# Kernel tuning notes

Hardware: AMD Instinct MI355X
Metric: run time of the kernel (lower is better)

## Reference

```python
import jax, jax.numpy as jnp
import numpy as np

N = 50000      # nodes
E = 250000     # edges
NG = 2500      # graphs
H = 32         # atom_dim
ND = 32        # node feature dim
ED = 16        # edge feature dim
CONV_N = 3     # message passing steps
EMB_STEPS = 3  # Set2Set processing steps


def setup_inputs() -> dict:
    key = jax.random.key(0)
    ks = jax.random.split(key, 16)
    w = lambda k, shape, s=0.05: jax.random.normal(k, shape, jnp.float32) * s
    return {
        "x": jax.random.normal(ks[0], (N, ND), jnp.float32),
        "edge_index": jax.random.randint(ks[1], (2, E), 0, N),
        "edge_attr": jax.random.normal(ks[2], (E, ED), jnp.float32),
        "batch": jnp.sort(jax.random.randint(ks[3], (N,), 0, NG)),
        "lin_w": w(ks[4], (ND, H)), "lin_b": jnp.zeros((H,), jnp.float32),
        "e_w1": w(ks[5], (ED, 2 * H)), "e_b1": jnp.zeros((2 * H,), jnp.float32),
        "e_w2": w(ks[6], (2 * H, H * H)), "e_b2": jnp.zeros((H * H,), jnp.float32),
        "gru_w_ih": w(ks[7], (3 * H, H)), "gru_w_hh": w(ks[8], (3 * H, H)),
        "gru_b_ih": jnp.zeros((3 * H,), jnp.float32), "gru_b_hh": jnp.zeros((3 * H,), jnp.float32),
        "lstm_w_ih": w(ks[9], (4 * H, 2 * H)), "lstm_w_hh": w(ks[10], (4 * H, H)),
        "lstm_b_ih": jnp.zeros((4 * H,), jnp.float32), "lstm_b_hh": jnp.zeros((4 * H,), jnp.float32),
        "pred_w": w(ks[11], (2 * H, 1)), "pred_b": jnp.zeros((1,), jnp.float32),
    }


def _mpnn_forward(x, edge_attr, lin_w, lin_b, e_w1, e_b1, e_w2, e_b2,
                  gru_w_ih, gru_w_hh, gru_b_ih, gru_b_hh,
                  lstm_w_ih, lstm_w_hh, lstm_b_ih, lstm_b_hh,
                  pred_w, pred_b, edge_index, batch):
    src, dst = edge_index[0], edge_index[1]
    # initial node embedding: relu(Linear(node_dim -> atom_dim))
    out = jax.nn.relu(x @ lin_w + lin_b)            # [N, H]
    h = out                                         # GRU hidden state [N, H]

    # edge-conditioned weights (edge MLP output is constant across conv steps)
    e_h = jax.nn.relu(edge_attr @ e_w1 + e_b1)      # [E, 2H]
    W_e = (e_h @ e_w2 + e_b2).reshape(E, H, H)      # [E, H, H]

    # mean-aggregation denominator per target node
    deg = jax.ops.segment_sum(jnp.ones((E,), out.dtype), dst, num_segments=N)
    denom = jnp.maximum(deg, 1.0)[:, None]          # [N, 1]

    for _ in range(CONV_N):
        # NNConv message: m_e = x_src @ W_e, mean-scattered to dst
        msg = jnp.einsum('eh,eho->eo', out[src], W_e)                   # [E, H]
        agg = jax.ops.segment_sum(msg, dst, num_segments=N) / denom     # [N, H]
        m = jax.nn.relu(agg)
        # single GRU cell step (seq_len=1)
        gi = m @ gru_w_ih.T + gru_b_ih              # [N, 3H]
        gh = h @ gru_w_hh.T + gru_b_hh              # [N, 3H]
        i_r, i_z, i_n = jnp.split(gi, 3, axis=-1)
        h_r, h_z, h_n = jnp.split(gh, 3, axis=-1)
        r = jax.nn.sigmoid(i_r + h_r)
        z = jax.nn.sigmoid(i_z + h_z)
        n = jnp.tanh(i_n + r * h_n)
        h = (1.0 - z) * n + z * h
        out = h

    # Set2Set pooling over graphs (only last embedding used, residual='last')
    q_star = jnp.zeros((NG, 2 * H), out.dtype)
    hl = jnp.zeros((NG, H), out.dtype)
    cl = jnp.zeros((NG, H), out.dtype)
    for _ in range(EMB_STEPS):
        g = q_star @ lstm_w_ih.T + lstm_b_ih + hl @ lstm_w_hh.T + lstm_b_hh  # [NG, 4H]
        gi_, gf_, gg_, go_ = jnp.split(g, 4, axis=-1)
        i_g = jax.nn.sigmoid(gi_)
        f_g = jax.nn.sigmoid(gf_)
        g_g = jnp.tanh(gg_)
        o_g = jax.nn.sigmoid(go_)
        cl = f_g * cl + i_g * g_g
        hl = o_g * jnp.tanh(cl)
        q = hl                                       # [NG, H]
        e = jnp.sum(out * q[batch], axis=-1)         # [N]
        e_max = jax.ops.segment_max(e, batch, num_segments=NG)
        e_exp = jnp.exp(e - e_max[batch])
        e_den = jax.ops.segment_sum(e_exp, batch, num_segments=NG)
        a = e_exp / e_den[batch]                     # softmax within each graph
        r_pool = jax.ops.segment_sum(a[:, None] * out, batch, num_segments=NG)  # [NG, H]
        q_star = jnp.concatenate([q, r_pool], axis=-1)

    pred = q_star @ pred_w + pred_b                  # [NG, 1]
    return pred.reshape(-1)


def reference(x, edge_index, edge_attr, batch, lin_w, lin_b, e_w1, e_b1, e_w2, e_b2,
              gru_w_ih, gru_w_hh, gru_b_ih, gru_b_hh,
              lstm_w_ih, lstm_w_hh, lstm_b_ih, lstm_b_hh, pred_w, pred_b):
    return _mpnn_forward(x, edge_attr, lin_w, lin_b, e_w1, e_b1, e_w2, e_b2,
                         gru_w_ih, gru_w_hh, gru_b_ih, gru_b_hh,
                         lstm_w_ih, lstm_w_hh, lstm_b_ih, lstm_b_hh,
                         pred_w, pred_b, edge_index, batch)
```

## Files before the change

### kernel.cpp

```cpp
#include <hip/hip_runtime.h>
#include <hip/hip_bf16.h>

namespace {
constexpr int kN = 50000;
constexpr int kE = 250000;
constexpr int kG = 2500;
constexpr int NB = 8;
constexpr int NBLK = (kN + 255) / 256;

__device__ __forceinline__ float sigmoidf_(float x) { return 1.0f / (1.0f + expf(-x)); }

__global__ void k_starts(const int* __restrict__ batch, int* __restrict__ starts) {
  int g = blockIdx.x * blockDim.x + threadIdx.x;
  if (g > kG) return;
  int lo = 0, hi = kN;
  while (lo < hi) {
    int mid = (lo + hi) >> 1;
    if (batch[mid] < g) lo = mid + 1; else hi = mid;
  }
  starts[g] = lo;
}

__global__ __launch_bounds__(256) void k_node_init(const float* __restrict__ x,
                                                   const float* __restrict__ lin_w,
                                                   const float* __restrict__ lin_b,
                                                   float* __restrict__ h) {
  __shared__ float ws[32 * 32];
  __shared__ float bs[32];
  for (int i = threadIdx.x; i < 1024; i += 256) ws[i] = lin_w[i];
  if (threadIdx.x < 32) bs[threadIdx.x] = lin_b[threadIdx.x];
  __syncthreads();
  int n = blockIdx.x * 256 + threadIdx.x;
  if (n >= kN) return;
  float xv[32];
  const float4* xp = (const float4*)(x + (size_t)n * 32);
#pragma unroll
  for (int i = 0; i < 8; ++i) {
    float4 v = xp[i];
    xv[4 * i + 0] = v.x; xv[4 * i + 1] = v.y; xv[4 * i + 2] = v.z; xv[4 * i + 3] = v.w;
  }
  float acc[32];
#pragma unroll
  for (int o = 0; o < 32; ++o) acc[o] = bs[o];
  for (int i = 0; i < 32; ++i) {
    float a = xv[i];
    const float4* wr = (const float4*)&ws[i * 32];
#pragma unroll
    for (int o4 = 0; o4 < 8; ++o4) {
      float4 w = wr[o4];
      acc[4 * o4 + 0] = fmaf(a, w.x, acc[4 * o4 + 0]);
      acc[4 * o4 + 1] = fmaf(a, w.y, acc[4 * o4 + 1]);
      acc[4 * o4 + 2] = fmaf(a, w.z, acc[4 * o4 + 2]);
      acc[4 * o4 + 3] = fmaf(a, w.w, acc[4 * o4 + 3]);
    }
  }
  float4* hp = (float4*)(h + (size_t)n * 32);
#pragma unroll
  for (int i = 0; i < 8; ++i) {
    float4 v;
    v.x = fmaxf(acc[4 * i + 0], 0.f);
    v.y = fmaxf(acc[4 * i + 1], 0.f);
    v.z = fmaxf(acc[4 * i + 2], 0.f);
    v.w = fmaxf(acc[4 * i + 3], 0.f);
    hp[i] = v;
  }
}

__global__ __launch_bounds__(256) void k_edge_h(const float* __restrict__ ea,
                                                const float* __restrict__ w1,
                                                const float* __restrict__ b1,
                                                const int* __restrict__ es_e,
                                                float* __restrict__ ehs) {
  __shared__ float ws[16 * 64];
  __shared__ float bs[64];
  for (int i = threadIdx.x; i < 1024; i += 256) ws[i] = w1[i];
  if (threadIdx.x < 64) bs[threadIdx.x] = b1[threadIdx.x];
  __syncthreads();
  int pos = blockIdx.x * 256 + threadIdx.x;
  if (pos >= kE) return;
  int e = es_e[pos];
  float av[16];
  const float4* ap = (const float4*)(ea + (size_t)e * 16);
#pragma unroll
  for (int i = 0; i < 4; ++i) {
    float4 v = ap[i];
    av[4 * i + 0] = v.x; av[4 * i + 1] = v.y; av[4 * i + 2] = v.z; av[4 * i + 3] = v.w;
  }
  float acc[64];
#pragma unroll
  for (int o = 0; o < 64; ++o) acc[o] = bs[o];
  for (int i = 0; i < 16; ++i) {
    float a = av[i];
    const float4* wr = (const float4*)&ws[i * 64];
#pragma unroll
    for (int o4 = 0; o4 < 16; ++o4) {
      float4 w = wr[o4];
      acc[4 * o4 + 0] = fmaf(a, w.x, acc[4 * o4 + 0]);
      acc[4 * o4 + 1] = fmaf(a, w.y, acc[4 * o4 + 1]);
      acc[4 * o4 + 2] = fmaf(a, w.z, acc[4 * o4 + 2]);
      acc[4 * o4 + 3] = fmaf(a, w.w, acc[4 * o4 + 3]);
    }
  }
  float4* op = (float4*)(ehs + (size_t)pos * 64);
#pragma unroll
  for (int i = 0; i < 16; ++i) {
    float4 v;
    v.x = fmaxf(acc[4 * i + 0], 0.f);
    v.y = fmaxf(acc[4 * i + 1], 0.f);
    v.z = fmaxf(acc[4 * i + 2], 0.f);
    v.w = fmaxf(acc[4 * i + 3], 0.f);
    op[i] = v;
  }
}

__global__ void k_hist2(const int* __restrict__ src, const int* __restrict__ dst,
                        int* __restrict__ cnt_s, int* __restrict__ cnt_d) {
  int e = blockIdx.x * blockDim.x + threadIdx.x;
  if (e < kE) {
    atomicAdd(&cnt_s[src[e]], 1);
    atomicAdd(&cnt_d[dst[e]], 1);
  }
}

__global__ __launch_bounds__(256) void k_scan_blk(const int* __restrict__ cnt_s, int* __restrict__ offs_s,
                                                  const int* __restrict__ cnt_d, int* __restrict__ offs_d,
                                                  int* __restrict__ part) {
  const int arr = blockIdx.y;
  const int* cnt = arr ? cnt_d : cnt_s;
  int* offs = arr ? offs_d : offs_s;
  __shared__ int wsum[4];
  const int i = blockIdx.x * 256 + threadIdx.x;
  const int lane = threadIdx.x & 63, wv = threadIdx.x >> 6;
  int v = (i < kN) ? cnt[i] : 0;
  int x = v;
#pragma unroll
  for (int d = 1; d < 64; d <<= 1) {
    int t = __shfl_up(x, d, 64);
    if (lane >= d) x += t;
  }
  if (lane == 63) wsum[wv] = x;
  __syncthreads();
  int pre = 0;
#pragma unroll
  for (int w = 0; w < 3; ++w) pre += (w < wv) ? wsum[w] : 0;
  if (i < kN) offs[i] = pre + x - v;
  if (threadIdx.x == 255) part[arr * 256 + blockIdx.x] = pre + x;
}

__global__ __launch_bounds__(256) void k_scan_part(int* __restrict__ part,
                                                   int* __restrict__ offs_s,
                                                   int* __restrict__ offs_d) {
  const int arr = blockIdx.x;
  int* p = part + arr * 256;
  __shared__ int wsum[4];
  const int i = threadIdx.x;
  const int lane = i & 63, wv = i >> 6;
  int v = (i < NBLK) ? p[i] : 0;
  int x = v;
#pragma unroll
  for (int d = 1; d < 64; d <<= 1) {
    int t = __shfl_up(x, d, 64);
    if (lane >= d) x += t;
  }
  if (lane == 63) wsum[wv] = x;
  __syncthreads();
  int pre = 0;
#pragma unroll
  for (int w = 0; w < 3; ++w) pre += (w < wv) ? wsum[w] : 0;
  if (i < NBLK) p[i] = pre + x - v;
  if (i == NBLK - 1) (arr ? offs_d : offs_s)[kN] = pre + x;
}

__global__ void k_scan_add(const int* __restrict__ part, int* __restrict__ offs_s,
                           int* __restrict__ offs_d) {
  const int arr = blockIdx.y;
  int* offs = arr ? offs_d : offs_s;
  int i = blockIdx.x * 256 + threadIdx.x;
  if (i < kN) offs[i] += part[arr * 256 + blockIdx.x];
}

__global__ void k_scatter(const int* __restrict__ src, const int* __restrict__ dst,
                          const int* __restrict__ offs_s, const int* __restrict__ offs_d,
                          int* __restrict__ cur_s, int* __restrict__ cur_d,
                          int* __restrict__ es_e, int* __restrict__ es_pk) {
  int e = blockIdx.x * blockDim.x + threadIdx.x;
  if (e >= kE) return;
  int s = src[e], d = dst[e];
  int pos = offs_s[s] + atomicAdd(&cur_s[s], 1);
  int pd = offs_d[d] + atomicAdd(&cur_d[d], 1);
  es_e[pos] = e;
  es_pk[pos] = pd | ((s & (NB - 1)) << 28);
}

__global__ void k_w2t(const float* __restrict__ w2, float* __restrict__ w2t) {
  int i = blockIdx.x * 256 + threadIdx.x;
  if (i >= 65536) return;
  int k = i & 63, oa = i >> 6;
  int o = oa & 31, a = oa >> 5;
  w2t[i] = w2[(size_t)k * 1024 + a * 32 + o];
}

__global__ __launch_bounds__(256, 4) void k_conv5(const float* __restrict__ h,
                                                  const float* __restrict__ ehs,
                                                  const float* __restrict__ w2t,
                                                  const float* __restrict__ b2,
                                                  const int* __restrict__ es_pk,
                                                  const int* __restrict__ offs,
                                                  float* __restrict__ msgbuf) {
  __shared__ float Ts[NB][32][36];
  __shared__ float hs[NB][32];
  __shared__ float hb2[NB][32];
  const int n0 = blockIdx.x * NB;
  const int t = threadIdx.x;
  const int nloc = t >> 5, o32 = t & 31;
  hs[nloc][o32] = h[(size_t)(n0 + nloc) * 32 + o32];
  __syncthreads();
  {
    float a0 = 0.f;
#pragma unroll 8
    for (int a = 0; a < 32; ++a) a0 = fmaf(hs[nloc][a], b2[a * 32 + o32], a0);
    hb2[nloc][o32] = a0;
  }
  const int og = t >> 3;
  const int kq = t & 7;
  const int es = offs[n0], ee = offs[n0 + NB];
  const float* wp = w2t + og * 64 + kq * 4;
  const int kg = t >> 5;

  for (int kh = 0; kh < 2; ++kh) {
    float4 acc[NB];
#pragma unroll
    for (int n = 0; n < NB; ++n) acc[n] = make_float4(0.f, 0.f, 0.f, 0.f);
    const float* wph = wp + kh * 32;
#pragma unroll 2
    for (int a4 = 0; a4 < 8; ++a4) {
      const float* wa = wph + (size_t)(a4 * 4) * 2048;
      float4 w0 = *(const float4*)(wa);
      float4 w1 = *(const float4*)(wa + 2048);
      float4 w2v = *(const float4*)(wa + 4096);
      float4 w3 = *(const float4*)(wa + 6144);
#pragma unroll
      for (int n = 0; n < NB; ++n) {
        float4 hv = *(const float4*)&hs[n][a4 * 4];
        acc[n].x = fmaf(hv.x, w0.x, acc[n].x); acc[n].y = fmaf(hv.x, w0.y, acc[n].y);
        acc[n].z = fmaf(hv.x, w0.z, acc[n].z); acc[n].w = fmaf(hv.x, w0.w, acc[n].w);
        acc[n].x = fmaf(hv.y, w1.x, acc[n].x); acc[n].y = fmaf(hv.y, w1.y, acc[n].y);
        acc[n].z = fmaf(hv.y, w1.z, acc[n].z); acc[n].w = fmaf(hv.y, w1.w, acc[n].w);
        acc[n].x = fmaf(hv.z, w2v.x, acc[n].x); acc[n].y = fmaf(hv.z, w2v.y, acc[n].y);
        acc[n].z = fmaf(hv.z, w2v.z, acc[n].z); acc[n].w = fmaf(hv.z, w2v.w, acc[n].w);
        acc[n].x = fmaf(hv.w, w3.x, acc[n].x); acc[n].y = fmaf(hv.w, w3.y, acc[n].y);
        acc[n].z = fmaf(hv.w, w3.z, acc[n].z); acc[n].w = fmaf(hv.w, w3.w, acc[n].w);
      }
    }
    if (kh) __syncthreads();
#pragma unroll
    for (int n = 0; n < NB; ++n) *(float4*)&Ts[n][og][kq * 4] = acc[n];
    __syncthreads();

    for (int ei = es + kg; ei < ee; ei += 8) {
      const int pk = es_pk[ei];
      const int nl = pk >> 28;
      const int pd = pk & 0x0FFFFFFF;
      const float* ehp = ehs + (size_t)ei * 64 + kh * 32;
      float m0 = kh ? msgbuf[(size_t)pd * 32 + o32] : hb2[nl][o32];
      float m1 = 0.f, m2 = 0.f, m3 = 0.f;
      const float* tp = &Ts[nl][o32][0];
#pragma unroll
      for (int kq2 = 0; kq2 < 8; ++kq2) {
        float4 eq = *(const float4*)(ehp + kq2 * 4);
        float4 tv = *(const float4*)(tp + kq2 * 4);
        m0 = fmaf(eq.x, tv.x, m0);
        m1 = fmaf(eq.y, tv.y, m1);
        m2 = fmaf(eq.z, tv.z, m2);
        m3 = fmaf(eq.w, tv.w, m3);
      }
      msgbuf[(size_t)pd * 32 + o32] = (m0 + m1) + (m2 + m3);
    }
  }
}

__global__ __launch_bounds__(256) void k_agg(const float* __restrict__ msgbuf,
                                             const int* __restrict__ offs_d,
                                             float* __restrict__ m_out) {
  int d = blockIdx.x * 8 + (threadIdx.x >> 5);
  if (d >= kN) return;
  int o = threadIdx.x & 31;
  int s = offs_d[d], e = offs_d[d + 1];
  float a0 = 0.f, a1 = 0.f;
  int j = s;
  for (; j + 1 < e; j += 2) {
    a0 += msgbuf[(size_t)j * 32 + o];
    a1 += msgbuf[(size_t)(j + 1) * 32 + o];
  }
  if (j < e) a0 += msgbuf[(size_t)j * 32 + o];
  float dn = (float)(e - s);
  if (dn < 1.f) dn = 1.f;
  m_out[(size_t)d * 32 + o] = fmaxf((a0 + a1) / dn, 0.f);
}

__global__ __launch_bounds__(256) void k_gru(float* __restrict__ h, const float* __restrict__ m_in,
                                             const float* __restrict__ Wih, const float* __restrict__ Whh,
                                             const float* __restrict__ bih, const float* __restrict__ bhh) {
  __shared__ float wih_s[96 * 32];
  __shared__ float whh_s[96 * 32];
  __shared__ float bih_s[96], bhh_s[96];
  for (int i = threadIdx.x; i < 96 * 32; i += 256) { wih_s[i] = Wih[i]; whh_s[i] = Whh[i]; }
  for (int i = threadIdx.x; i < 96; i += 256) { bih_s[i] = bih[i]; bhh_s[i] = bhh[i]; }
  __syncthreads();
  int n = blockIdx.x * 256 + threadIdx.x;
  if (n >= kN) return;
  float m[32], hv[32];
  const float4* ap = (const float4*)(m_in + (size_t)n * 32);
  const float4* hp = (const float4*)(h + (size_t)n * 32);
#pragma unroll
  for (int i = 0; i < 8; ++i) {
    float4 a = ap[i];
    m[4 * i + 0] = a.x; m[4 * i + 1] = a.y; m[4 * i + 2] = a.z; m[4 * i + 3] = a.w;
    float4 b = hp[i];
    hv[4 * i + 0] = b.x; hv[4 * i + 1] = b.y; hv[4 * i + 2] = b.z; hv[4 * i + 3] = b.w;
  }
  float rr[32], zz[32];
#pragma unroll 4
  for (int j = 0; j < 32; ++j) {
    float accA = bih_s[j], accB = bhh_s[j];
    const float4* wi = (const float4*)&wih_s[j * 32];
    const float4* wh = (const float4*)&whh_s[j * 32];
#pragma unroll
    for (int i = 0; i < 8; ++i) {
      float4 a = wi[i], b = wh[i];
      accA = fmaf(m[4 * i + 0], a.x, accA); accA = fmaf(m[4 * i + 1], a.y, accA);
      accA = fmaf(m[4 * i + 2], a.z, accA); accA = fmaf(m[4 * i + 3], a.w, accA);
      accB = fmaf(hv[4 * i + 0], b.x, accB); accB = fmaf(hv[4 * i + 1], b.y, accB);
      accB = fmaf(hv[4 * i + 2], b.z, accB); accB = fmaf(hv[4 * i + 3], b.w, accB);
    }
    rr[j] = sigmoidf_(accA + accB);
  }
#pragma unroll 4
  for (int j = 0; j < 32; ++j) {
    int row = 32 + j;
    float accA = bih_s[row], accB = bhh_s[row];
    const float4* wi = (const float4*)&wih_s[row * 32];
    const float4* wh = (const float4*)&whh_s[row * 32];
#pragma unroll
    for (int i = 0; i < 8; ++i) {
      float4 a = wi[i], b = wh[i];
      accA = fmaf(m[4 * i + 0], a.x, accA); accA = fmaf(m[4 * i + 1], a.y, accA);
      accA = fmaf(m[4 * i + 2], a.z, accA); accA = fmaf(m[4 * i + 3], a.w, accA);
      accB = fmaf(hv[4 * i + 0], b.x, accB); accB = fmaf(hv[4 * i + 1], b.y, accB);
      accB = fmaf(hv[4 * i + 2], b.z, accB); accB = fmaf(hv[4 * i + 3], b.w, accB);
    }
    zz[j] = sigmoidf_(accA + accB);
  }
#pragma unroll 4
  for (int j = 0; j < 32; ++j) {
    int row = 64 + j;
    float accA = bih_s[row], accB = bhh_s[row];
    const float4* wi = (const float4*)&wih_s[row * 32];
    const float4* wh = (const float4*)&whh_s[row * 32];
#pragma unroll
    for (int i = 0; i < 8; ++i) {
      float4 a = wi[i], b = wh[i];
      accA = fmaf(m[4 * i + 0], a.x, accA); accA = fmaf(m[4 * i + 1], a.y, accA);
      accA = fmaf(m[4 * i + 2], a.z, accA); accA = fmaf(m[4 * i + 3], a.w, accA);
      accB = fmaf(hv[4 * i + 0], b.x, accB); accB = fmaf(hv[4 * i + 1], b.y, accB);
      accB = fmaf(hv[4 * i + 2], b.z, accB); accB = fmaf(hv[4 * i + 3], b.w, accB);
    }
    float ng = tanhf(accA + rr[j] * accB);
    zz[j] = (1.f - zz[j]) * ng + zz[j] * hv[j];
  }
  float4* hw = (float4*)(h + (size_t)n * 32);
#pragma unroll
  for (int i = 0; i < 8; ++i)
    hw[i] = make_float4(zz[4 * i + 0], zz[4 * i + 1], zz[4 * i + 2], zz[4 * i + 3]);
}

__global__ __launch_bounds__(256) void k_s2s(const float* __restrict__ h,
                                             const int* __restrict__ starts,
                                             const float* __restrict__ lwih,
                                             const float* __restrict__ lwhh,
                                             const float* __restrict__ lbih,
                                             const float* __restrict__ lbhh,
                                             const float* __restrict__ pw,
                                             const float* __restrict__ pb,
                                             float* __restrict__ out) {
  __shared__ float wih_s[128][65];
  __shared__ float whh_s[128][33];
  __shared__ float bsum[128];
  for (int i = threadIdx.x; i < 128 * 64; i += 256) wih_s[i >> 6][i & 63] = lwih[i];
  for (int i = threadIdx.x; i < 128 * 32; i += 256) whh_s[i >> 5][i & 31] = lwhh[i];
  for (int i = threadIdx.x; i < 128; i += 256) bsum[i] = lbih[i] + lbhh[i];
  __syncthreads();
  const int g = blockIdx.x * 4 + (threadIdx.x >> 6);
  if (g >= kG) return;
  const int lane = threadIdx.x & 63;
  const int o = lane & 31;
  const int r1 = lane, r2 = lane + 64;
  const int s = starts[g], e = starts[g + 1];
  float c = 0.f, hl = 0.f, rp = 0.f;
  for (int step = 0; step < 3; ++step) {
    float v1 = bsum[r1], v2 = bsum[r2];
    for (int i = 0; i < 32; ++i) {
      float hli = __shfl(hl, i, 64);
      float rpi = __shfl(rp, i, 64);
      v1 = fmaf(wih_s[r1][i], hli, v1);
      v1 = fmaf(wih_s[r1][32 + i], rpi, v1);
      v1 = fmaf(whh_s[r1][i], hli, v1);
      v2 = fmaf(wih_s[r2][i], hli, v2);
      v2 = fmaf(wih_s[r2][32 + i], rpi, v2);
      v2 = fmaf(whh_s[r2][i], hli, v2);
    }
    float fg = sigmoidf_(__shfl(v1, 32 + o, 64));
    float og_ = sigmoidf_(__shfl(v2, 32 + o, 64));
    float ig = sigmoidf_(v1);
    float gg = tanhf(v2);
    c = fg * c + ig * gg;
    hl = og_ * tanhf(c);
    float q = __shfl(hl, o, 64);
    float mx = -3.0e38f;
    for (int nn = s; nn < e; nn += 2) {
      int n = nn + (lane >> 5);
      float val = (n < e) ? h[(size_t)n * 32 + o] * q : 0.f;
#pragma unroll
      for (int d = 16; d; d >>= 1) val += __shfl_xor(val, d, 32);
      if (n < e) mx = fmaxf(mx, val);
    }
    mx = fmaxf(mx, __shfl_xor(mx, 32, 64));
    float den = 0.f, racc = 0.f;
    for (int nn = s; nn < e; nn += 2) {
      int n = nn + (lane >> 5);
      float hvo = 0.f, val = 0.f;
      if (n < e) { hvo = h[(size_t)n * 32 + o]; val = hvo * q; }
#pragma unroll
      for (int d = 16; d; d >>= 1) val += __shfl_xor(val, d, 32);
      if (n < e) { float p = expf(val - mx); den += p; racc = fmaf(p, hvo, racc); }
    }
    den += __shfl_xor(den, 32, 64);
    racc += __shfl_xor(racc, 32, 64);
    rp = (e > s) ? racc / den : 0.f;
  }
  float acc = __shfl(hl, o, 64) * pw[o] + rp * pw[32 + o];
#pragma unroll
  for (int d = 16; d; d >>= 1) acc += __shfl_xor(acc, d, 32);
  if (lane == 0) out[g] = acc + pb[0];
}

}

extern "C" void kernel_launch(void* const* d_in, const int* in_sizes, int n_in,
                              void* d_out, int out_size, void* d_ws, size_t ws_size,
                              hipStream_t stream) {
  const float* x     = (const float*)d_in[0];
  const int*   eidx  = (const int*)d_in[1];
  const float* eattr = (const float*)d_in[2];
  const int*   batch = (const int*)d_in[3];
  const float* lin_w = (const float*)d_in[4];
  const float* lin_b = (const float*)d_in[5];
  const float* e_w1  = (const float*)d_in[6];
  const float* e_b1  = (const float*)d_in[7];
  const float* e_w2  = (const float*)d_in[8];
  const float* e_b2  = (const float*)d_in[9];
  const float* gwih  = (const float*)d_in[10];
  const float* gwhh  = (const float*)d_in[11];
  const float* gbih  = (const float*)d_in[12];
  const float* gbhh  = (const float*)d_in[13];
  const float* lwih  = (const float*)d_in[14];
  const float* lwhh  = (const float*)d_in[15];
  const float* lbih  = (const float*)d_in[16];
  const float* lbhh  = (const float*)d_in[17];
  const float* pw    = (const float*)d_in[18];
  const float* pb    = (const float*)d_in[19];
  const int* srcp = eidx;
  const int* dstp = eidx + kE;

  float* ws = (float*)d_ws;
  size_t off = 0;
  auto alloc = [&](size_t nel) {
    float* p = ws + off;
    off += (nel + 255) & ~(size_t)255;
    return p;
  };
  float* hbuf   = alloc((size_t)kN * 32);
  float* mbuf   = alloc((size_t)kN * 32);
  float* ehs    = alloc((size_t)kE * 64);
  float* msgbuf = alloc((size_t)kE * 32);
  float* w2t    = alloc(65536);
  int* starts   = (int*)alloc(kG + 1);
  int* cnt_s    = (int*)alloc(kN);
  int* cnt_d    = (int*)alloc(kN);
  int* cur_s    = (int*)alloc(kN);
  int* cur_d    = (int*)alloc(kN);
  int* offs_s   = (int*)alloc(kN + 1);
  int* offs_d   = (int*)alloc(kN + 1);
  int* es_e     = (int*)alloc(kE);
  int* es_pk    = (int*)alloc(kE);
  int* part     = (int*)alloc(512);
  if (ws_size / 4 < off) return;

  hipMemsetAsync(cnt_s, 0, (size_t)((cur_d + ((kN + 255) & ~255)) - cnt_s) * 4, stream);

  k_starts<<<(kG + 1 + 255) / 256, 256, 0, stream>>>(batch, starts);
  k_node_init<<<(kN + 255) / 256, 256, 0, stream>>>(x, lin_w, lin_b, hbuf);
  k_hist2<<<(kE + 255) / 256, 256, 0, stream>>>(srcp, dstp, cnt_s, cnt_d);
  {
    dim3 g(NBLK, 2);
    k_scan_blk<<<g, 256, 0, stream>>>(cnt_s, offs_s, cnt_d, offs_d, part);
    k_scan_part<<<2, 256, 0, stream>>>(part, offs_s, offs_d);
    k_scan_add<<<g, 256, 0, stream>>>(part, offs_s, offs_d);
  }
  k_scatter<<<(kE + 255) / 256, 256, 0, stream>>>(srcp, dstp, offs_s, offs_d, cur_s, cur_d,
                                                  es_e, es_pk);
  k_edge_h<<<(kE + 255) / 256, 256, 0, stream>>>(eattr, e_w1, e_b1, es_e, ehs);
  k_w2t<<<65536 / 256, 256, 0, stream>>>(e_w2, w2t);

  for (int step = 0; step < 3; ++step) {
    k_conv5<<<kN / NB, 256, 0, stream>>>(hbuf, ehs, w2t, e_b2, es_pk, offs_s, msgbuf);
    k_agg<<<(kN + 7) / 8, 256, 0, stream>>>(msgbuf, offs_d, mbuf);
    k_gru<<<(kN + 255) / 256, 256, 0, stream>>>(hbuf, mbuf, gwih, gwhh, gbih, gbhh);
  }

  k_s2s<<<(kG + 3) / 4, 256, 0, stream>>>(hbuf, starts, lwih, lwhh, lbih, lbhh, pw, pb,
                                          (float*)d_out);
}
```

Baseline: 915.8 us.

## Fuse aggregation into GRU and merge small setup kernels

Aggregation of per-edge messages now happens inside the GRU kernel: each block reduces incoming messages for its 256 nodes into shared memory and then runs the GRU update, removing the intermediate mbuf round trip and one launch per step. The node init and degree histogram are merged into one launch, and the graph-start search and w2 transpose are folded into the scan-add kernel, cutting several launches. The cost is that the aggregation grid drops from about 6250 blocks to about 196, and shared memory per block rises, which may lower parallelism during the gather phase.

```diff
diff --git a/kernel.cpp b/kernel.cpp
--- a/kernel.cpp
+++ b/kernel.cpp
@@ -7,24 +7,26 @@
 constexpr int kG = 2500;
 constexpr int NB = 8;
 constexpr int NBLK = (kN + 255) / 256;
+constexpr int EBLK = (kE + 255) / 256;
 
 __device__ __forceinline__ float sigmoidf_(float x) { return 1.0f / (1.0f + expf(-x)); }
 
-__global__ void k_starts(const int* __restrict__ batch, int* __restrict__ starts) {
-  int g = blockIdx.x * blockDim.x + threadIdx.x;
-  if (g > kG) return;
-  int lo = 0, hi = kN;
-  while (lo < hi) {
-    int mid = (lo + hi) >> 1;
-    if (batch[mid] < g) lo = mid + 1; else hi = mid;
-  }
-  starts[g] = lo;
-}
-
-__global__ __launch_bounds__(256) void k_node_init(const float* __restrict__ x,
+__global__ __launch_bounds__(256) void k_init_hist(const float* __restrict__ x,
                                                    const float* __restrict__ lin_w,
                                                    const float* __restrict__ lin_b,
-                                                   float* __restrict__ h) {
+                                                   float* __restrict__ h,
+                                                   const int* __restrict__ src,
+                                                   const int* __restrict__ dst,
+                                                   int* __restrict__ cnt_s,
+                                                   int* __restrict__ cnt_d) {
+  if (blockIdx.x >= NBLK) {
+    int e = (blockIdx.x - NBLK) * 256 + threadIdx.x;
+    if (e < kE) {
+      atomicAdd(&cnt_s[src[e]], 1);
+      atomicAdd(&cnt_d[dst[e]], 1);
+    }
+    return;
+  }
   __shared__ float ws[32 * 32];
   __shared__ float bs[32];
   for (int i = threadIdx.x; i < 1024; i += 256) ws[i] = lin_w[i];
@@ -110,15 +112,6 @@
     v.z = fmaxf(acc[4 * i + 2], 0.f);
     v.w = fmaxf(acc[4 * i + 3], 0.f);
     op[i] = v;
-  }
-}
-
-__global__ void k_hist2(const int* __restrict__ src, const int* __restrict__ dst,
-                        int* __restrict__ cnt_s, int* __restrict__ cnt_d) {
-  int e = blockIdx.x * blockDim.x + threadIdx.x;
-  if (e < kE) {
-    atomicAdd(&cnt_s[src[e]], 1);
-    atomicAdd(&cnt_d[dst[e]], 1);
   }
 }
 
@@ -172,11 +165,30 @@
 }
 
 __global__ void k_scan_add(const int* __restrict__ part, int* __restrict__ offs_s,
-                           int* __restrict__ offs_d) {
+                           int* __restrict__ offs_d, const int* __restrict__ batch,
+                           int* __restrict__ starts, const float* __restrict__ w2,
+                           float* __restrict__ w2t) {
   const int arr = blockIdx.y;
   int* offs = arr ? offs_d : offs_s;
   int i = blockIdx.x * 256 + threadIdx.x;
   if (i < kN) offs[i] += part[arr * 256 + blockIdx.x];
+  if (arr == 0 && blockIdx.x < 10) {
+    int g = blockIdx.x * 256 + threadIdx.x;
+    if (g <= kG) {
+      int lo = 0, hi = kN;
+      while (lo < hi) {
+        int mid = (lo + hi) >> 1;
+        if (batch[mid] < g) lo = mid + 1; else hi = mid;
+      }
+      starts[g] = lo;
+    }
+  }
+  int gid = (arr * gridDim.x + blockIdx.x) * 256 + threadIdx.x;
+  if (gid < 65536) {
+    int k = gid & 63, oa = gid >> 6;
+    int o = oa & 31, a = oa >> 5;
+    w2t[gid] = w2[(size_t)k * 1024 + a * 32 + o];
+  }
 }
 
 __global__ void k_scatter(const int* __restrict__ src, const int* __restrict__ dst,
@@ -190,14 +202,6 @@
   int pd = offs_d[d] + atomicAdd(&cur_d[d], 1);
   es_e[pos] = e;
   es_pk[pos] = pd | ((s & (NB - 1)) << 28);
-}
-
-__global__ void k_w2t(const float* __restrict__ w2, float* __restrict__ w2t) {
-  int i = blockIdx.x * 256 + threadIdx.x;
-  if (i >= 65536) return;
-  int k = i & 63, oa = i >> 6;
-  int o = oa & 31, a = oa >> 5;
-  w2t[i] = w2[(size_t)k * 1024 + a * 32 + o];
 }
 
 __global__ __launch_bounds__(256, 4) void k_conv5(const float* __restrict__ h,
@@ -279,43 +283,47 @@
   }
 }
 
-__global__ __launch_bounds__(256) void k_agg(const float* __restrict__ msgbuf,
-                                             const int* __restrict__ offs_d,
-                                             float* __restrict__ m_out) {
-  int d = blockIdx.x * 8 + (threadIdx.x >> 5);
-  if (d >= kN) return;
-  int o = threadIdx.x & 31;
-  int s = offs_d[d], e = offs_d[d + 1];
-  float a0 = 0.f, a1 = 0.f;
-  int j = s;
-  for (; j + 1 < e; j += 2) {
-    a0 += msgbuf[(size_t)j * 32 + o];
-    a1 += msgbuf[(size_t)(j + 1) * 32 + o];
-  }
-  if (j < e) a0 += msgbuf[(size_t)j * 32 + o];
-  float dn = (float)(e - s);
-  if (dn < 1.f) dn = 1.f;
-  m_out[(size_t)d * 32 + o] = fmaxf((a0 + a1) / dn, 0.f);
-}
-
-__global__ __launch_bounds__(256) void k_gru(float* __restrict__ h, const float* __restrict__ m_in,
-                                             const float* __restrict__ Wih, const float* __restrict__ Whh,
-                                             const float* __restrict__ bih, const float* __restrict__ bhh) {
+__global__ __launch_bounds__(256) void k_aggru(const float* __restrict__ msgbuf,
+                                               const int* __restrict__ offs_d,
+                                               float* __restrict__ h,
+                                               const float* __restrict__ Wih,
+                                               const float* __restrict__ Whh,
+                                               const float* __restrict__ bih,
+                                               const float* __restrict__ bhh) {
+  __shared__ float m_s[256][33];
   __shared__ float wih_s[96 * 32];
   __shared__ float whh_s[96 * 32];
   __shared__ float bih_s[96], bhh_s[96];
   for (int i = threadIdx.x; i < 96 * 32; i += 256) { wih_s[i] = Wih[i]; whh_s[i] = Whh[i]; }
   for (int i = threadIdx.x; i < 96; i += 256) { bih_s[i] = bih[i]; bhh_s[i] = bhh[i]; }
-  __syncthreads();
-  int n = blockIdx.x * 256 + threadIdx.x;
+  const int grp = threadIdx.x >> 5, o = threadIdx.x & 31;
+  const int nbase = blockIdx.x * 256;
+  for (int j = 0; j < 32; ++j) {
+    int dl = grp * 32 + j;
+    int d = nbase + dl;
+    if (d < kN) {
+      int s = offs_d[d], e = offs_d[d + 1];
+      float a0 = 0.f, a1 = 0.f;
+      int jj = s;
+      for (; jj + 1 < e; jj += 2) {
+        a0 += msgbuf[(size_t)jj * 32 + o];
+        a1 += msgbuf[(size_t)(jj + 1) * 32 + o];
+      }
+      if (jj < e) a0 += msgbuf[(size_t)jj * 32 + o];
+      float dn = (float)(e - s);
+      if (dn < 1.f) dn = 1.f;
+      m_s[dl][o] = fmaxf((a0 + a1) / dn, 0.f);
+    }
+  }
+  __syncthreads();
+  const int n = nbase + threadIdx.x;
   if (n >= kN) return;
   float m[32], hv[32];
-  const float4* ap = (const float4*)(m_in + (size_t)n * 32);
   const float4* hp = (const float4*)(h + (size_t)n * 32);
 #pragma unroll
+  for (int i = 0; i < 32; ++i) m[i] = m_s[threadIdx.x][i];
+#pragma unroll
   for (int i = 0; i < 8; ++i) {
-    float4 a = ap[i];
-    m[4 * i + 0] = a.x; m[4 * i + 1] = a.y; m[4 * i + 2] = a.z; m[4 * i + 3] = a.w;
     float4 b = hp[i];
     hv[4 * i + 0] = b.x; hv[4 * i + 1] = b.y; hv[4 * i + 2] = b.z; hv[4 * i + 3] = b.w;
   }
@@ -480,7 +488,6 @@
     return p;
   };
   float* hbuf   = alloc((size_t)kN * 32);
-  float* mbuf   = alloc((size_t)kN * 32);
   float* ehs    = alloc((size_t)kE * 64);
   float* msgbuf = alloc((size_t)kE * 32);
   float* w2t    = alloc(65536);
@@ -498,24 +505,19 @@
 
   hipMemsetAsync(cnt_s, 0, (size_t)((cur_d + ((kN + 255) & ~255)) - cnt_s) * 4, stream);
 
-  k_starts<<<(kG + 1 + 255) / 256, 256, 0, stream>>>(batch, starts);
-  k_node_init<<<(kN + 255) / 256, 256, 0, stream>>>(x, lin_w, lin_b, hbuf);
-  k_hist2<<<(kE + 255) / 256, 256, 0, stream>>>(srcp, dstp, cnt_s, cnt_d);
+  k_init_hist<<<NBLK + EBLK, 256, 0, stream>>>(x, lin_w, lin_b, hbuf, srcp, dstp, cnt_s, cnt_d);
   {
     dim3 g(NBLK, 2);
     k_scan_blk<<<g, 256, 0, stream>>>(cnt_s, offs_s, cnt_d, offs_d, part);
     k_scan_part<<<2, 256, 0, stream>>>(part, offs_s, offs_d);
-    k_scan_add<<<g, 256, 0, stream>>>(part, offs_s, offs_d);
-  }
-  k_scatter<<<(kE + 255) / 256, 256, 0, stream>>>(srcp, dstp, offs_s, offs_d, cur_s, cur_d,
-                                                  es_e, es_pk);
-  k_edge_h<<<(kE + 255) / 256, 256, 0, stream>>>(eattr, e_w1, e_b1, es_e, ehs);
-  k_w2t<<<65536 / 256, 256, 0, stream>>>(e_w2, w2t);
+    k_scan_add<<<g, 256, 0, stream>>>(part, offs_s, offs_d, batch, starts, e_w2, w2t);
+  }
+  k_scatter<<<EBLK, 256, 0, stream>>>(srcp, dstp, offs_s, offs_d, cur_s, cur_d, es_e, es_pk);
+  k_edge_h<<<EBLK, 256, 0, stream>>>(eattr, e_w1, e_b1, es_e, ehs);
 
   for (int step = 0; step < 3; ++step) {
     k_conv5<<<kN / NB, 256, 0, stream>>>(hbuf, ehs, w2t, e_b2, es_pk, offs_s, msgbuf);
-    k_agg<<<(kN + 7) / 8, 256, 0, stream>>>(msgbuf, offs_d, mbuf);
-    k_gru<<<(kN + 255) / 256, 256, 0, stream>>>(hbuf, mbuf, gwih, gwhh, gbih, gbhh);
+    k_aggru<<<NBLK, 256, 0, stream>>>(msgbuf, offs_d, hbuf, gwih, gwhh, gbih, gbhh);
   }
 
   k_s2s<<<(kG + 3) / 4, 256, 0, stream>>>(hbuf, starts, lwih, lwhh, lbih, lbhh, pw, pb,
```

After: 1.015 ms. +10.9%, slower.
